# Optimization experiments

Hardware: AMD Instinct MI355X
Metric: run time of the kernel (lower is better)

Reference implementation:

```python
import jax, jax.numpy as jnp
import numpy as np

TEMP = 0.5  # temperature
UNITS = [512, 256, 128]
B, M, D, C = 256, 512, 512, 8


def setup_inputs() -> dict:
    key = jax.random.key(0)
    ks = jax.random.split(key, 9)
    inp = {}
    inp["ec_output"] = jax.random.normal(ks[0], (B, M, D), jnp.float32)
    inp["mask"] = jax.random.randint(ks[1], (B, 1, 1, M), 0, 2).astype(jnp.float32)
    inp["label"] = jax.random.randint(ks[2], (B, C), 0, 2)
    dims = [D] + UNITS
    for i in range(3):
        fan_in = dims[i]
        inp[f"W{i+1}"] = jax.random.normal(ks[3 + i], (C, dims[i], dims[i + 1]), jnp.float32) * (1.0 / np.sqrt(fan_in))
        inp[f"b{i+1}"] = jnp.zeros((C, dims[i + 1]), jnp.float32)
    return inp


def reference(ec_output, mask, label, W1, b1, W2, b2, W3, b3):
    # masked sum pooling: mask==0 means keep (as in the TF code)
    m = (jnp.squeeze(mask) == 0).astype(ec_output.dtype)  # (B, M)
    pooled = jnp.einsum('bmd,bm->bd', ec_output, m)        # (B, D)

    # per-class 3-layer relu MLP, batched over class axis c
    h = jax.nn.relu(jnp.einsum('bd,cde->cbe', pooled, W1) + b1[:, None, :])
    h = jax.nn.relu(jnp.einsum('cbe,cef->cbf', h, W2) + b2[:, None, :])
    h = jax.nn.relu(jnp.einsum('cbf,cfg->cbg', h, W3) + b3[:, None, :])

    # tf.math.l2_normalize semantics
    z = h * jax.lax.rsqrt(jnp.maximum(jnp.sum(h * h, axis=-1, keepdims=True), 1e-12))  # (C, B, u)

    # supervised contrastive loss per class (training=True path)
    lab = label.T.astype(z.dtype)                 # (C, B)
    mask1 = (lab == 1).astype(z.dtype)
    mask0 = (lab == 0).astype(z.dtype)
    num_p = jnp.sum(mask1, axis=1, keepdims=True)  # (C, 1)
    num_n = jnp.sum(mask0, axis=1, keepdims=True)
    num_vec = num_p * mask1 + num_n * mask0        # (C, B)

    ip = jnp.einsum('cbe,cke->cbk', z, z)          # (C, B, B)
    ip = ip * (1.0 - jnp.eye(B, dtype=z.dtype)) / TEMP

    denom = num_vec * jnp.log(jnp.sum(jnp.exp(ip), axis=2))  # (C, B)
    numer = mask1 * jnp.einsum('cbk,ck->cb', ip, mask1) + mask0 * jnp.einsum('cbk,ck->cb', ip, mask0)
    losses = -jnp.sum((numer - denom) / num_vec, axis=1)      # (C,)

    return z, losses
```

## Files before the change

kernel.cpp:

```cpp
#include <hip/hip_runtime.h>
#include <hip/hip_bf16.h>

typedef unsigned short u16;
typedef __bf16 bf16x8 __attribute__((ext_vector_type(8)));
typedef float f32x4 __attribute__((ext_vector_type(4)));


__device__ __forceinline__ float bf2f(u16 u) {
    union { float f; unsigned int i; } x; x.i = ((unsigned int)u) << 16; return x.f;
}
__device__ __forceinline__ u16 f2bf(float f) {
    union { float f; unsigned int i; } x; x.f = f;
    unsigned int r = x.i + 0x7FFFu + ((x.i >> 16) & 1u);
    return (u16)(r >> 16);
}

__global__ __launch_bounds__(1024) void pool_kernel(
    const u16* __restrict__ ec, const u16* __restrict__ mask,
    u16* __restrict__ pooled)
{
    int b = blockIdx.x, tid = threadIdx.x;
    __shared__ float wm[512];
    __shared__ float red[16][512];
    if (tid < 512)
        wm[tid] = (bf2f(mask[b * 512 + tid]) == 0.0f) ? 1.0f : 0.0f;
    __syncthreads();
    int g = tid & 63, mo = tid >> 6;
    float acc[8];
    #pragma unroll
    for (int j = 0; j < 8; j++) acc[j] = 0.0f;
    const u16* base = ec + (size_t)b * 512 * 512;
    for (int m = mo; m < 512; m += 16) {
        if (wm[m] != 0.0f) {
            union { uint4 v; u16 s[8]; } u;
            u.v = *(const uint4*)&base[(size_t)m * 512 + g * 8];
            #pragma unroll
            for (int j = 0; j < 8; j++) acc[j] += bf2f(u.s[j]);
        }
    }
    #pragma unroll
    for (int j = 0; j < 8; j++) red[mo][g * 8 + j] = acc[j];
    __syncthreads();
    if (tid < 512) {
        float s = 0.0f;
        #pragma unroll
        for (int k = 0; k < 16; k++) s += red[k][tid];
        pooled[(size_t)b * 512 + tid] = f2bf(s);
    }
}

__global__ __launch_bounds__(256) void mlp_gemm64(
    const u16* __restrict__ A, const u16* __restrict__ W,
    const u16* __restrict__ bias, u16* __restrict__ out,
    int K, int N, int aBatch, int mtiles, int ntiles)
{
    int bid = blockIdx.x;
    int per_c = mtiles * ntiles;
    int c = bid / per_c, rem = bid % per_c;
    int mt = rem / ntiles, nt = rem % ntiles;
    const u16* aBase = A + (size_t)c * aBatch + (size_t)mt * 64 * K;
    const u16* wBase = W + (size_t)c * K * N + nt * 64;
    __shared__ __align__(16) u16 As[2][64][72];
    __shared__ __align__(16) u16 Bs[2][64][72];
    int tid = threadIdx.x;
    int w = tid >> 6, l15 = tid & 15, q = (tid >> 4) & 3;
    int r0 = tid >> 3, kc0 = tid & 7;
    int r1 = (tid + 256) >> 3, kc1 = tid & 7;
    f32x4 acc[4];
    #pragma unroll
    for (int t = 0; t < 4; t++)
        #pragma unroll
        for (int e = 0; e < 4; e++) acc[t][e] = 0.0f;

    uint4 aReg[2], wReg[2];
    aReg[0] = *(const uint4*)&aBase[(size_t)r0 * K + kc0 * 8];
    aReg[1] = *(const uint4*)&aBase[(size_t)r1 * K + kc1 * 8];
    wReg[0] = *(const uint4*)&wBase[(size_t)r0 * N + kc0 * 8];
    wReg[1] = *(const uint4*)&wBase[(size_t)r1 * N + kc1 * 8];

    int nIter = K >> 6;
    for (int it = 0; it < nIter; ++it) {
        int cur = it & 1;
        *(uint4*)&As[cur][r0][kc0 * 8] = aReg[0];
        *(uint4*)&As[cur][r1][kc1 * 8] = aReg[1];
        {
            union { uint4 v; u16 s[8]; } u; u.v = wReg[0];
            #pragma unroll
            for (int j = 0; j < 8; j++) Bs[cur][kc0 * 8 + j][r0] = u.s[j];
        }
        {
            union { uint4 v; u16 s[8]; } u; u.v = wReg[1];
            #pragma unroll
            for (int j = 0; j < 8; j++) Bs[cur][kc1 * 8 + j][r1] = u.s[j];
        }
        if (it + 1 < nIter) {
            int k0n = (it + 1) * 64;
            aReg[0] = *(const uint4*)&aBase[(size_t)r0 * K + k0n + kc0 * 8];
            aReg[1] = *(const uint4*)&aBase[(size_t)r1 * K + k0n + kc1 * 8];
            wReg[0] = *(const uint4*)&wBase[(size_t)(k0n + r0) * N + kc0 * 8];
            wReg[1] = *(const uint4*)&wBase[(size_t)(k0n + r1) * N + kc1 * 8];
        }
        __syncthreads();
        #pragma unroll
        for (int ks = 0; ks < 64; ks += 32) {
            bf16x8 av = *(const bf16x8*)&As[cur][w * 16 + l15][ks + q * 8];
            #pragma unroll
            for (int t = 0; t < 4; t++) {
                bf16x8 bv = *(const bf16x8*)&Bs[cur][t * 16 + l15][ks + q * 8];
                acc[t] = __builtin_amdgcn_mfma_f32_16x16x32_bf16(av, bv, acc[t], 0, 0, 0);
            }
        }
    }
    #pragma unroll
    for (int t = 0; t < 4; t++) {
        int col = nt * 64 + t * 16 + l15;
        float bv = bf2f(bias[c * N + col]);
        #pragma unroll
        for (int r = 0; r < 4; r++) {
            int row = mt * 64 + w * 16 + q * 4 + r;
            float v = acc[t][r] + bv;
            v = v > 0.0f ? v : 0.0f;
            out[((size_t)c * 256 + row) * N + col] = f2bf(v);
        }
    }
}

__global__ __launch_bounds__(256) void mlp_gemm3_norm(
    const u16* __restrict__ A, const u16* __restrict__ W,
    const u16* __restrict__ bias, float* __restrict__ zout, u16* __restrict__ zbf)
{
    const int K = 256, N = 128;
    int bid = blockIdx.x;
    int c = bid >> 4, mt = bid & 15;
    const u16* aBase = A + ((size_t)c * 256 + mt * 16) * K;
    const u16* wBase = W + (size_t)c * K * N;
    __shared__ __align__(16) u16 As[16][72];
    __shared__ __align__(16) u16 Bs[128][72];
    __shared__ float ssq_s[4][16];
    __shared__ float scale_s[16];
    int tid = threadIdx.x;
    int w = tid >> 6, l15 = tid & 15, q = (tid >> 4) & 3;
    f32x4 acc[2];
    #pragma unroll
    for (int t = 0; t < 2; t++)
        #pragma unroll
        for (int e = 0; e < 4; e++) acc[t][e] = 0.0f;

    for (int k0 = 0; k0 < K; k0 += 64) {
        if (tid < 128) {
            int r = tid >> 3, kc = tid & 7;
            *(uint4*)&As[r][kc * 8] = *(const uint4*)&aBase[(size_t)r * K + k0 + kc * 8];
        }
        #pragma unroll
        for (int i = 0; i < 4; i++) {
            int idx = tid + i * 256;
            int kk = idx >> 4, n8 = (idx & 15) * 8;
            union { uint4 v; u16 s[8]; } u;
            u.v = *(const uint4*)&wBase[(size_t)(k0 + kk) * N + n8];
            #pragma unroll
            for (int j = 0; j < 8; j++) Bs[n8 + j][kk] = u.s[j];
        }
        __syncthreads();
        #pragma unroll
        for (int ks = 0; ks < 64; ks += 32) {
            bf16x8 av = *(const bf16x8*)&As[l15][ks + q * 8];
            #pragma unroll
            for (int t = 0; t < 2; t++) {
                bf16x8 bv = *(const bf16x8*)&Bs[w * 32 + t * 16 + l15][ks + q * 8];
                acc[t] = __builtin_amdgcn_mfma_f32_16x16x32_bf16(av, bv, acc[t], 0, 0, 0);
            }
        }
        __syncthreads();
    }
    float val[2][4];
    float ssq[4] = {0.f, 0.f, 0.f, 0.f};
    #pragma unroll
    for (int t = 0; t < 2; t++) {
        float bv = bf2f(bias[c * N + w * 32 + t * 16 + l15]);
        #pragma unroll
        for (int r = 0; r < 4; r++) {
            float v = acc[t][r] + bv;
            v = v > 0.0f ? v : 0.0f;
            val[t][r] = v;
            ssq[r] += v * v;
        }
    }
    #pragma unroll
    for (int off = 1; off < 16; off <<= 1)
        #pragma unroll
        for (int r = 0; r < 4; r++) ssq[r] += __shfl_xor(ssq[r], off);
    if (l15 == 0) {
        #pragma unroll
        for (int r = 0; r < 4; r++) ssq_s[w][q * 4 + r] = ssq[r];
    }
    __syncthreads();
    if (tid < 16) {
        float s = ssq_s[0][tid] + ssq_s[1][tid] + ssq_s[2][tid] + ssq_s[3][tid];
        scale_s[tid] = rsqrtf(fmaxf(s, 1e-12f));
    }
    __syncthreads();
    #pragma unroll
    for (int t = 0; t < 2; t++)
        #pragma unroll
        for (int r = 0; r < 4; r++) {
            int row = mt * 16 + q * 4 + r;
            int col = w * 32 + t * 16 + l15;
            float zv = val[t][r] * scale_s[q * 4 + r];
            size_t o = ((size_t)c * 256 + row) * 128 + col;
            zout[o] = zv;
            zbf[o] = f2bf(zv);
        }
}

__global__ __launch_bounds__(256) void contrast_partial(
    const u16* __restrict__ z, const int* __restrict__ label,
    float* __restrict__ rws, float* __restrict__ s1ws, float* __restrict__ s0ws)
{
    int bid = blockIdx.x;
    int c = bid >> 4, rem = bid & 15;
    int bt = rem >> 2, kt = rem & 3;
    __shared__ __align__(16) u16 Zb[64][136];
    __shared__ __align__(16) u16 Zk[64][136];
    __shared__ float lm1[64];
    int tid = threadIdx.x;
    int w = tid >> 6, l15 = tid & 15, q = (tid >> 4) & 3;
    const u16* zc = z + (size_t)c * 256 * 128;
    #pragma unroll
    for (int i = 0; i < 4; i++) {
        int idx = tid + i * 256; int r = idx >> 4, kc = idx & 15;
        *(uint4*)&Zb[r][kc * 8] = *(const uint4*)&zc[(size_t)(bt * 64 + r) * 128 + kc * 8];
        *(uint4*)&Zk[r][kc * 8] = *(const uint4*)&zc[(size_t)(kt * 64 + r) * 128 + kc * 8];
    }
    if (tid < 64) lm1[tid] = (label[(kt * 64 + tid) * 8 + c] == 1) ? 1.0f : 0.0f;
    __syncthreads();

    f32x4 acc[4];
    #pragma unroll
    for (int t = 0; t < 4; t++)
        #pragma unroll
        for (int e = 0; e < 4; e++) acc[t][e] = 0.0f;
    #pragma unroll
    for (int ks = 0; ks < 128; ks += 32) {
        bf16x8 av = *(const bf16x8*)&Zb[w * 16 + l15][ks + q * 8];
        #pragma unroll
        for (int t = 0; t < 4; t++) {
            bf16x8 bv = *(const bf16x8*)&Zk[t * 16 + l15][ks + q * 8];
            acc[t] = __builtin_amdgcn_mfma_f32_16x16x32_bf16(av, bv, acc[t], 0, 0, 0);
        }
    }
    float pr[4] = {0.f,0.f,0.f,0.f}, p1[4] = {0.f,0.f,0.f,0.f}, p0[4] = {0.f,0.f,0.f,0.f};
    #pragma unroll
    for (int t = 0; t < 4; t++) {
        int kl = t * 16 + l15;
        int kkg = kt * 64 + kl;
        float m1 = lm1[kl];
        #pragma unroll
        for (int r = 0; r < 4; r++) {
            int rbg = bt * 64 + w * 16 + q * 4 + r;
            float v = (rbg == kkg) ? 0.0f : acc[t][r] * 2.0f;
            pr[r] += __expf(v);
            p1[r] += v * m1;
            p0[r] += v * (1.0f - m1);
        }
    }
    #pragma unroll
    for (int off = 1; off < 16; off <<= 1)
        #pragma unroll
        for (int r = 0; r < 4; r++) {
            pr[r] += __shfl_xor(pr[r], off);
            p1[r] += __shfl_xor(p1[r], off);
            p0[r] += __shfl_xor(p0[r], off);
        }
    if (l15 == 0) {
        #pragma unroll
        for (int r = 0; r < 4; r++) {
            int rbg = bt * 64 + w * 16 + q * 4 + r;
            atomicAdd(&rws[c * 256 + rbg], pr[r]);
            atomicAdd(&s1ws[c * 256 + rbg], p1[r]);
            atomicAdd(&s0ws[c * 256 + rbg], p0[r]);
        }
    }
}

__global__ __launch_bounds__(256) void loss_kernel(
    const int* __restrict__ label, const float* __restrict__ rws,
    const float* __restrict__ s1ws, const float* __restrict__ s0ws,
    float* __restrict__ lout)
{
    int c = blockIdx.x, b = threadIdx.x;
    __shared__ float sh[256];
    int lab = label[b * 8 + c];
    float m1 = (lab == 1) ? 1.0f : 0.0f;
    sh[b] = m1;
    __syncthreads();
    for (int s = 128; s > 0; s >>= 1) {
        if (b < s) sh[b] += sh[b + s];
        __syncthreads();
    }
    float num_p = sh[0];
    __syncthreads();
    float num_n = 256.0f - num_p;
    float num_vec = (m1 > 0.0f) ? num_p : num_n;
    float numer = (m1 > 0.0f) ? s1ws[c * 256 + b] : s0ws[c * 256 + b];
    float term = numer / num_vec - __logf(rws[c * 256 + b]);
    sh[b] = term;
    __syncthreads();
    for (int s = 128; s > 0; s >>= 1) {
        if (b < s) sh[b] += sh[b + s];
        __syncthreads();
    }
    if (b == 0) lout[c] = -sh[0];
}

extern "C" void kernel_launch(void* const* d_in, const int* in_sizes, int n_in,
                              void* d_out, int out_size, void* d_ws, size_t ws_size,
                              hipStream_t stream) {
    (void)in_sizes; (void)n_in; (void)ws_size;
    const u16* ec   = (const u16*)d_in[0];
    const u16* mask = (const u16*)d_in[1];
    const int* label = (const int*)d_in[2];
    const u16* W1 = (const u16*)d_in[3];
    const u16* b1 = (const u16*)d_in[4];
    const u16* W2 = (const u16*)d_in[5];
    const u16* b2 = (const u16*)d_in[6];
    const u16* W3 = (const u16*)d_in[7];
    const u16* b3 = (const u16*)d_in[8];
    float* zout = (float*)d_out;
    char* ws = (char*)d_ws;
    u16* pooled = (u16*)(ws + 0);
    u16* h1     = (u16*)(ws + 262144);
    u16* h2     = (u16*)(ws + 2359296);
    u16* zbf    = (u16*)(ws + 3407872);
    float* rws  = (float*)(ws + 3932160);
    float* s1ws = rws + 2048;
    float* s0ws = rws + 4096;

    hipMemsetAsync(rws, 0, 3 * 2048 * sizeof(float), stream);
    pool_kernel<<<256, 1024, 0, stream>>>(ec, mask, pooled);
    mlp_gemm64<<<256, 256, 0, stream>>>(pooled, W1, b1, h1, 512, 512, 0, 4, 8);
    mlp_gemm64<<<128, 256, 0, stream>>>(h1, W2, b2, h2, 512, 256, 256 * 512, 4, 4);
    mlp_gemm3_norm<<<128, 256, 0, stream>>>(h2, W3, b3, zout, zbf);
    contrast_partial<<<128, 256, 0, stream>>>(zbf, label, rws, s1ws, s0ws);
    loss_kernel<<<8, 256, 0, stream>>>(label, rws, s1ws, s0ws, zout + (out_size - 8));
}
```

Before: 381.7 us.

## Fuse contrastive partial and loss kernels; widen MLP GEMM blocks to 512 threads

Merges the contrast-partial and loss kernels into one per-class kernel with 1024 threads. It keeps all of z for a class in shared memory and reduces in shared memory, so the workspace memset and the global atomics go away. The MLP GEMM kernel now uses 8 waves per 64x64 tile, each wave computing a 16x32 sub-tile. This cuts launch count and atomic traffic, but runs the contrast stage on only 8 blocks and uses much more shared memory per block.

```diff
diff --git a/kernel.cpp b/kernel.cpp
--- a/kernel.cpp
+++ b/kernel.cpp
@@ -49,7 +49,7 @@
     }
 }
 
-__global__ __launch_bounds__(256) void mlp_gemm64(
+__global__ __launch_bounds__(512) void mlp_gemm64(
     const u16* __restrict__ A, const u16* __restrict__ W,
     const u16* __restrict__ bias, u16* __restrict__ out,
     int K, int N, int aBatch, int mtiles, int ntiles)
@@ -64,60 +64,50 @@
     __shared__ __align__(16) u16 Bs[2][64][72];
     int tid = threadIdx.x;
     int w = tid >> 6, l15 = tid & 15, q = (tid >> 4) & 3;
+    int wm = w >> 1, wn = w & 1;
     int r0 = tid >> 3, kc0 = tid & 7;
-    int r1 = (tid + 256) >> 3, kc1 = tid & 7;
-    f32x4 acc[4];
-    #pragma unroll
-    for (int t = 0; t < 4; t++)
+    f32x4 acc[2];
+    #pragma unroll
+    for (int t = 0; t < 2; t++)
         #pragma unroll
         for (int e = 0; e < 4; e++) acc[t][e] = 0.0f;
 
-    uint4 aReg[2], wReg[2];
-    aReg[0] = *(const uint4*)&aBase[(size_t)r0 * K + kc0 * 8];
-    aReg[1] = *(const uint4*)&aBase[(size_t)r1 * K + kc1 * 8];
-    wReg[0] = *(const uint4*)&wBase[(size_t)r0 * N + kc0 * 8];
-    wReg[1] = *(const uint4*)&wBase[(size_t)r1 * N + kc1 * 8];
+    uint4 aReg, wReg;
+    aReg = *(const uint4*)&aBase[(size_t)r0 * K + kc0 * 8];
+    wReg = *(const uint4*)&wBase[(size_t)r0 * N + kc0 * 8];
 
     int nIter = K >> 6;
     for (int it = 0; it < nIter; ++it) {
         int cur = it & 1;
-        *(uint4*)&As[cur][r0][kc0 * 8] = aReg[0];
-        *(uint4*)&As[cur][r1][kc1 * 8] = aReg[1];
+        *(uint4*)&As[cur][r0][kc0 * 8] = aReg;
         {
-            union { uint4 v; u16 s[8]; } u; u.v = wReg[0];
+            union { uint4 v; u16 s[8]; } u; u.v = wReg;
             #pragma unroll
             for (int j = 0; j < 8; j++) Bs[cur][kc0 * 8 + j][r0] = u.s[j];
-        }
-        {
-            union { uint4 v; u16 s[8]; } u; u.v = wReg[1];
-            #pragma unroll
-            for (int j = 0; j < 8; j++) Bs[cur][kc1 * 8 + j][r1] = u.s[j];
         }
         if (it + 1 < nIter) {
             int k0n = (it + 1) * 64;
-            aReg[0] = *(const uint4*)&aBase[(size_t)r0 * K + k0n + kc0 * 8];
-            aReg[1] = *(const uint4*)&aBase[(size_t)r1 * K + k0n + kc1 * 8];
-            wReg[0] = *(const uint4*)&wBase[(size_t)(k0n + r0) * N + kc0 * 8];
-            wReg[1] = *(const uint4*)&wBase[(size_t)(k0n + r1) * N + kc1 * 8];
+            aReg = *(const uint4*)&aBase[(size_t)r0 * K + k0n + kc0 * 8];
+            wReg = *(const uint4*)&wBase[(size_t)(k0n + r0) * N + kc0 * 8];
         }
         __syncthreads();
         #pragma unroll
         for (int ks = 0; ks < 64; ks += 32) {
-            bf16x8 av = *(const bf16x8*)&As[cur][w * 16 + l15][ks + q * 8];
-            #pragma unroll
-            for (int t = 0; t < 4; t++) {
-                bf16x8 bv = *(const bf16x8*)&Bs[cur][t * 16 + l15][ks + q * 8];
+            bf16x8 av = *(const bf16x8*)&As[cur][wm * 16 + l15][ks + q * 8];
+            #pragma unroll
+            for (int t = 0; t < 2; t++) {
+                bf16x8 bv = *(const bf16x8*)&Bs[cur][wn * 32 + t * 16 + l15][ks + q * 8];
                 acc[t] = __builtin_amdgcn_mfma_f32_16x16x32_bf16(av, bv, acc[t], 0, 0, 0);
             }
         }
     }
     #pragma unroll
-    for (int t = 0; t < 4; t++) {
-        int col = nt * 64 + t * 16 + l15;
+    for (int t = 0; t < 2; t++) {
+        int col = nt * 64 + wn * 32 + t * 16 + l15;
         float bv = bf2f(bias[c * N + col]);
         #pragma unroll
         for (int r = 0; r < 4; r++) {
-            int row = mt * 64 + w * 16 + q * 4 + r;
+            int row = mt * 64 + wm * 16 + q * 4 + r;
             float v = acc[t][r] + bv;
             v = v > 0.0f ? v : 0.0f;
             out[((size_t)c * 256 + row) * N + col] = f2bf(v);
@@ -212,104 +202,121 @@
         }
 }
 
-__global__ __launch_bounds__(256) void contrast_partial(
+__global__ __launch_bounds__(1024) void contrast_loss(
     const u16* __restrict__ z, const int* __restrict__ label,
-    float* __restrict__ rws, float* __restrict__ s1ws, float* __restrict__ s0ws)
+    float* __restrict__ losses)
 {
-    int bid = blockIdx.x;
-    int c = bid >> 4, rem = bid & 15;
-    int bt = rem >> 2, kt = rem & 3;
-    __shared__ __align__(16) u16 Zb[64][136];
-    __shared__ __align__(16) u16 Zk[64][136];
-    __shared__ float lm1[64];
+    int c = blockIdx.x;
     int tid = threadIdx.x;
     int w = tid >> 6, l15 = tid & 15, q = (tid >> 4) & 3;
+    int rw = w >> 2, cw = w & 3;
+    __shared__ __align__(16) u16 Zk[256][136];
+    __shared__ float lm1[256];
+    __shared__ float npw[16];
+    __shared__ float pr_s[4][256];
+    __shared__ float p1_s[4][256];
+    __shared__ float p0_s[4][256];
+    __shared__ float term_s[256];
+    __shared__ float red4[4];
+
     const u16* zc = z + (size_t)c * 256 * 128;
     #pragma unroll
     for (int i = 0; i < 4; i++) {
-        int idx = tid + i * 256; int r = idx >> 4, kc = idx & 15;
-        *(uint4*)&Zb[r][kc * 8] = *(const uint4*)&zc[(size_t)(bt * 64 + r) * 128 + kc * 8];
-        *(uint4*)&Zk[r][kc * 8] = *(const uint4*)&zc[(size_t)(kt * 64 + r) * 128 + kc * 8];
-    }
-    if (tid < 64) lm1[tid] = (label[(kt * 64 + tid) * 8 + c] == 1) ? 1.0f : 0.0f;
-    __syncthreads();
-
-    f32x4 acc[4];
-    #pragma unroll
-    for (int t = 0; t < 4; t++)
-        #pragma unroll
-        for (int e = 0; e < 4; e++) acc[t][e] = 0.0f;
+        int idx = tid + i * 1024;
+        int r = idx >> 4, kc = idx & 15;
+        *(uint4*)&Zk[r][kc * 8] = *(const uint4*)&zc[(size_t)r * 128 + kc * 8];
+    }
+    float m1 = 0.0f;
+    if (tid < 256) {
+        m1 = (label[tid * 8 + c] == 1) ? 1.0f : 0.0f;
+        lm1[tid] = m1;
+    }
+    float nps = m1;
+    #pragma unroll
+    for (int off = 1; off < 64; off <<= 1) nps += __shfl_xor(nps, off);
+    if ((tid & 63) == 0) npw[w] = nps;
+    __syncthreads();
+
+    f32x4 acc[4][4];
+    #pragma unroll
+    for (int a = 0; a < 4; a++)
+        #pragma unroll
+        for (int t = 0; t < 4; t++)
+            #pragma unroll
+            for (int e = 0; e < 4; e++) acc[a][t][e] = 0.0f;
     #pragma unroll
     for (int ks = 0; ks < 128; ks += 32) {
-        bf16x8 av = *(const bf16x8*)&Zb[w * 16 + l15][ks + q * 8];
+        bf16x8 av[4], bv[4];
+        #pragma unroll
+        for (int a = 0; a < 4; a++)
+            av[a] = *(const bf16x8*)&Zk[rw * 64 + a * 16 + l15][ks + q * 8];
+        #pragma unroll
+        for (int t = 0; t < 4; t++)
+            bv[t] = *(const bf16x8*)&Zk[cw * 64 + t * 16 + l15][ks + q * 8];
+        #pragma unroll
+        for (int a = 0; a < 4; a++)
+            #pragma unroll
+            for (int t = 0; t < 4; t++)
+                acc[a][t] = __builtin_amdgcn_mfma_f32_16x16x32_bf16(av[a], bv[t], acc[a][t], 0, 0, 0);
+    }
+    #pragma unroll
+    for (int a = 0; a < 4; a++) {
+        float pr[4] = {0.f, 0.f, 0.f, 0.f};
+        float p1[4] = {0.f, 0.f, 0.f, 0.f};
+        float p0[4] = {0.f, 0.f, 0.f, 0.f};
         #pragma unroll
         for (int t = 0; t < 4; t++) {
-            bf16x8 bv = *(const bf16x8*)&Zk[t * 16 + l15][ks + q * 8];
-            acc[t] = __builtin_amdgcn_mfma_f32_16x16x32_bf16(av, bv, acc[t], 0, 0, 0);
-        }
-    }
-    float pr[4] = {0.f,0.f,0.f,0.f}, p1[4] = {0.f,0.f,0.f,0.f}, p0[4] = {0.f,0.f,0.f,0.f};
-    #pragma unroll
-    for (int t = 0; t < 4; t++) {
-        int kl = t * 16 + l15;
-        int kkg = kt * 64 + kl;
-        float m1 = lm1[kl];
-        #pragma unroll
-        for (int r = 0; r < 4; r++) {
-            int rbg = bt * 64 + w * 16 + q * 4 + r;
-            float v = (rbg == kkg) ? 0.0f : acc[t][r] * 2.0f;
-            pr[r] += __expf(v);
-            p1[r] += v * m1;
-            p0[r] += v * (1.0f - m1);
-        }
-    }
-    #pragma unroll
-    for (int off = 1; off < 16; off <<= 1)
-        #pragma unroll
-        for (int r = 0; r < 4; r++) {
-            pr[r] += __shfl_xor(pr[r], off);
-            p1[r] += __shfl_xor(p1[r], off);
-            p0[r] += __shfl_xor(p0[r], off);
-        }
-    if (l15 == 0) {
-        #pragma unroll
-        for (int r = 0; r < 4; r++) {
-            int rbg = bt * 64 + w * 16 + q * 4 + r;
-            atomicAdd(&rws[c * 256 + rbg], pr[r]);
-            atomicAdd(&s1ws[c * 256 + rbg], p1[r]);
-            atomicAdd(&s0ws[c * 256 + rbg], p0[r]);
-        }
-    }
-}
-
-__global__ __launch_bounds__(256) void loss_kernel(
-    const int* __restrict__ label, const float* __restrict__ rws,
-    const float* __restrict__ s1ws, const float* __restrict__ s0ws,
-    float* __restrict__ lout)
-{
-    int c = blockIdx.x, b = threadIdx.x;
-    __shared__ float sh[256];
-    int lab = label[b * 8 + c];
-    float m1 = (lab == 1) ? 1.0f : 0.0f;
-    sh[b] = m1;
-    __syncthreads();
-    for (int s = 128; s > 0; s >>= 1) {
-        if (b < s) sh[b] += sh[b + s];
-        __syncthreads();
-    }
-    float num_p = sh[0];
-    __syncthreads();
-    float num_n = 256.0f - num_p;
-    float num_vec = (m1 > 0.0f) ? num_p : num_n;
-    float numer = (m1 > 0.0f) ? s1ws[c * 256 + b] : s0ws[c * 256 + b];
-    float term = numer / num_vec - __logf(rws[c * 256 + b]);
-    sh[b] = term;
-    __syncthreads();
-    for (int s = 128; s > 0; s >>= 1) {
-        if (b < s) sh[b] += sh[b + s];
-        __syncthreads();
-    }
-    if (b == 0) lout[c] = -sh[0];
+            int kbg = cw * 64 + t * 16 + l15;
+            float mm = lm1[kbg];
+            #pragma unroll
+            for (int r = 0; r < 4; r++) {
+                int rbg = rw * 64 + a * 16 + q * 4 + r;
+                float v = (rbg == kbg) ? 0.0f : acc[a][t][r] * 2.0f;
+                pr[r] += __expf(v);
+                p1[r] += v * mm;
+                p0[r] += v * (1.0f - mm);
+            }
+        }
+        #pragma unroll
+        for (int off = 1; off < 16; off <<= 1)
+            #pragma unroll
+            for (int r = 0; r < 4; r++) {
+                pr[r] += __shfl_xor(pr[r], off);
+                p1[r] += __shfl_xor(p1[r], off);
+                p0[r] += __shfl_xor(p0[r], off);
+            }
+        if (l15 == 0) {
+            #pragma unroll
+            for (int r = 0; r < 4; r++) {
+                int rbg = rw * 64 + a * 16 + q * 4 + r;
+                pr_s[cw][rbg] = pr[r];
+                p1_s[cw][rbg] = p1[r];
+                p0_s[cw][rbg] = p0[r];
+            }
+        }
+    }
+    __syncthreads();
+    if (tid < 256) {
+        float rt = pr_s[0][tid] + pr_s[1][tid] + pr_s[2][tid] + pr_s[3][tid];
+        float s1 = p1_s[0][tid] + p1_s[1][tid] + p1_s[2][tid] + p1_s[3][tid];
+        float s0 = p0_s[0][tid] + p0_s[1][tid] + p0_s[2][tid] + p0_s[3][tid];
+        float np = 0.0f;
+        #pragma unroll
+        for (int k = 0; k < 16; k++) np += npw[k];
+        float m = lm1[tid];
+        float num_vec = (m > 0.0f) ? np : 256.0f - np;
+        float numer = (m > 0.0f) ? s1 : s0;
+        term_s[tid] = numer / num_vec - __logf(rt);
+    }
+    __syncthreads();
+    if (tid < 256) {
+        float t4 = term_s[tid];
+        #pragma unroll
+        for (int off = 1; off < 64; off <<= 1) t4 += __shfl_xor(t4, off);
+        if ((tid & 63) == 0) red4[w] = t4;
+    }
+    __syncthreads();
+    if (tid == 0) losses[c] = -(red4[0] + red4[1] + red4[2] + red4[3]);
 }
 
 extern "C" void kernel_launch(void* const* d_in, const int* in_sizes, int n_in,
@@ -331,15 +338,10 @@
     u16* h1     = (u16*)(ws + 262144);
     u16* h2     = (u16*)(ws + 2359296);
     u16* zbf    = (u16*)(ws + 3407872);
-    float* rws  = (float*)(ws + 3932160);
-    float* s1ws = rws + 2048;
-    float* s0ws = rws + 4096;
-
-    hipMemsetAsync(rws, 0, 3 * 2048 * sizeof(float), stream);
+
     pool_kernel<<<256, 1024, 0, stream>>>(ec, mask, pooled);
-    mlp_gemm64<<<256, 256, 0, stream>>>(pooled, W1, b1, h1, 512, 512, 0, 4, 8);
-    mlp_gemm64<<<128, 256, 0, stream>>>(h1, W2, b2, h2, 512, 256, 256 * 512, 4, 4);
+    mlp_gemm64<<<256, 512, 0, stream>>>(pooled, W1, b1, h1, 512, 512, 0, 4, 8);
+    mlp_gemm64<<<128, 512, 0, stream>>>(h1, W2, b2, h2, 512, 256, 256 * 512, 4, 4);
     mlp_gemm3_norm<<<128, 256, 0, stream>>>(h2, W3, b3, zout, zbf);
-    contrast_partial<<<128, 256, 0, stream>>>(zbf, label, rws, s1ws, s0ws);
-    loss_kernel<<<8, 256, 0, stream>>>(label, rws, s1ws, s0ws, zout + (out_size - 8));
-}
+    contrast_loss<<<8, 1024, 0, stream>>>(zbf, label, zout + (out_size - 8));
+}
```

New measurement: 380.6 us. About the same (-0.3%).
